# Kernel optimization log

Measured on AMD Instinct MI355X. Metric: run time of the kernel, lower is better.

## Reference

```python
import jax, jax.numpy as jnp
import numpy as np

N, E, F = 20000, 320000, 128
H = 2 * F  # MLP width = 256
EPS = 1e-5
TANH_ALPHA = 1.0


def setup_inputs() -> dict:
    key = jax.random.key(0)
    ks = jax.random.split(key, 16)
    x = jax.random.normal(ks[0], (N, F), dtype=jnp.float32)
    edge_index = jax.random.randint(ks[1], (2, E), 0, N, dtype=jnp.int64)
    s = 1.0 / np.sqrt(H)
    W1 = jax.random.uniform(ks[2], (H, H), jnp.float32, -s, s)
    b1 = jax.random.uniform(ks[3], (H,), jnp.float32, -s, s)
    g1 = jnp.ones((H,), jnp.float32)
    be1 = jnp.zeros((H,), jnp.float32)
    rm1 = jax.random.normal(ks[4], (H,), jnp.float32) * 0.1
    rv1 = jax.random.uniform(ks[5], (H,), jnp.float32, 0.5, 1.5)
    W2 = jax.random.uniform(ks[6], (H, H), jnp.float32, -s, s)
    b2 = jax.random.uniform(ks[7], (H,), jnp.float32, -s, s)
    g2 = jnp.ones((H,), jnp.float32)
    be2 = jnp.zeros((H,), jnp.float32)
    rm2 = jax.random.normal(ks[8], (H,), jnp.float32) * 0.1
    rv2 = jax.random.uniform(ks[9], (H,), jnp.float32, 0.5, 1.5)
    W3 = jax.random.uniform(ks[10], (F, H), jnp.float32, -s, s)
    b3 = jax.random.uniform(ks[11], (F,), jnp.float32, -s, s)
    return {"x": x, "edge_index": edge_index,
            "W1": W1, "b1": b1, "g1": g1, "be1": be1, "rm1": rm1, "rv1": rv1,
            "W2": W2, "b2": b2, "g2": g2, "be2": be2, "rm2": rm2, "rv2": rv2,
            "W3": W3, "b3": b3}


def _block(h, W, b, g, be, rm, rv):
    # Linear -> (Dropout inactive at eval) -> BatchNorm1d (eval, running stats) -> ReLU
    h = h @ W.T + b
    h = (h - rm) * (g * jax.lax.rsqrt(rv + EPS)) + be
    return jax.nn.relu(h)


def reference(x, edge_index, W1, b1, g1, be1, rm1, rv1,
              W2, b2, g2, be2, rm2, rv2, W3, b3):
    src, dst = edge_index[0], edge_index[1]  # PyG: x_j = x[src], x_i = x[dst]
    xi = x[dst]                              # [E, F]
    xj = x[src]                              # [E, F]
    h = jnp.concatenate([xi, xj - xi], axis=-1)  # [E, 2F]
    h = _block(h, W1, b1, g1, be1, rm1, rv1)
    h = _block(h, W2, b2, g2, be2, rm2, rv2)
    h = h @ W3.T + b3                        # [E, F]
    # scatter-mean aggregation over destination nodes
    summed = jax.ops.segment_sum(h, dst, num_segments=N)              # [N, F]
    cnt = jax.ops.segment_sum(jnp.ones((E,), h.dtype), dst, num_segments=N)
    agg = summed / jnp.maximum(cnt, 1.0)[:, None]
    return jnp.tanh(TANH_ALPHA * agg)
```

## Files before the change

kernel.cpp:

```cpp
#include <hip/hip_runtime.h>
#include <math.h>

#define NN 20000
#define EE 320000
#define FF 128
#define HH 256
#define MT 128

typedef _Float16 f16x8 __attribute__((ext_vector_type(8)));
typedef _Float16 f16x4 __attribute__((ext_vector_type(4)));
typedef float    f32x4  __attribute__((ext_vector_type(4)));
typedef float    f32x16 __attribute__((ext_vector_type(16)));

#define HADDR(m, bcol) (((m) << 9) + ((bcol) ^ (((m) & 7) << 4)))

#define WPTR_OFF  80000
#define SPAIR_OFF 160000
#define W2F_OFF   6560000
#define W3F_OFF   6691072
#define WCF_OFF   6756608
#define PQ_OFF    6887680

#define PB_HIST 1250
#define PB_W2   32
#define PB_WC   32
#define PB_W3   16
#define PREP_BLOCKS (PB_HIST + PB_W2 + PB_WC + PB_W3)

#define NODEB 313


__global__ __launch_bounds__(256) void prep_kernel(
    const int* __restrict__ eidx,
    const float* __restrict__ W1, const float* __restrict__ W2,
    const float* __restrict__ W3,
    _Float16* __restrict__ w2f, _Float16* __restrict__ wcf,
    _Float16* __restrict__ w3f, int* __restrict__ cnt)
{
    const int b = blockIdx.x, t = threadIdx.x;
    if (b < PB_HIST) {
        const int e = b * 256 + t;
        atomicAdd(&cnt[eidx[EE + e]], 1);
    } else if (b < PB_HIST + PB_W2) {
        const int f = (b - PB_HIST) * 256 + t;
        const int n = ((f >> 10) << 5) | (f & 31);
        const int k = (((f >> 6) & 15) << 4) | (((f >> 5) & 1) << 3);
        const float* s = W2 + (size_t)n * HH + k;
        _Float16 o[8];
        #pragma unroll
        for (int j = 0; j < 8; ++j) o[j] = (_Float16)s[j];
        __builtin_memcpy(w2f + (size_t)f * 8, o, 16);
    } else if (b < PB_HIST + PB_W2 + PB_WC) {
        const int f = (b - (PB_HIST + PB_W2)) * 256 + t;
        const int n = ((f >> 8) << 4) | (f & 15);
        const int k = (((f >> 6) & 3) << 5) | (((f >> 4) & 3) << 3);
        _Float16 o[8];
        if (n < HH) {
            const float* a = W1 + (size_t)n * HH + k;
            #pragma unroll
            for (int j = 0; j < 8; ++j) o[j] = (_Float16)(a[j] - a[FF + j]);
        } else {
            const float* a = W1 + (size_t)(n - HH) * HH + FF + k;
            #pragma unroll
            for (int j = 0; j < 8; ++j) o[j] = (_Float16)a[j];
        }
        __builtin_memcpy(wcf + (size_t)f * 8, o, 16);
    } else {
        const int f = (b - (PB_HIST + PB_W2 + PB_WC)) * 256 + t;
        const int n = ((f >> 10) << 5) | (f & 31);
        const int k = (((f >> 6) & 15) << 4) | (((f >> 5) & 1) << 3);
        const float* s = W3 + (size_t)n * HH + k;
        _Float16 o[8];
        #pragma unroll
        for (int j = 0; j < 8; ++j) o[j] = (_Float16)s[j];
        __builtin_memcpy(w3f + (size_t)f * 8, o, 16);
    }
}

__global__ __launch_bounds__(512) void node_kernel(
    const float* __restrict__ x, const _Float16* __restrict__ wcf,
    const float* __restrict__ b1, const float* __restrict__ g1,
    const float* __restrict__ be1, const float* __restrict__ rm1,
    const float* __restrict__ rv1,
    _Float16* __restrict__ PQ,
    const int* __restrict__ cnt, int* __restrict__ wptr)
{
    if (blockIdx.x == NODEB) {
        __shared__ int sp[512];
        const int t = threadIdx.x;
        const int base = t * 40;
        int s = 0;
        #pragma unroll 1
        for (int g = 0; g < 5; ++g) {
            int v[8];
            #pragma unroll
            for (int u = 0; u < 8; ++u) {
                const int idx = base + g * 8 + u;
                v[u] = (idx < NN) ? cnt[idx] : 0;
            }
            #pragma unroll
            for (int u = 0; u < 8; ++u) s += v[u];
        }
        sp[t] = s;
        __syncthreads();
        for (int d = 1; d < 512; d <<= 1) {
            const int v = (t >= d) ? sp[t - d] : 0;
            __syncthreads();
            sp[t] += v;
            __syncthreads();
        }
        int run = sp[t] - s;
        #pragma unroll 1
        for (int g = 0; g < 5; ++g) {
            int v[8];
            #pragma unroll
            for (int u = 0; u < 8; ++u) {
                const int idx = base + g * 8 + u;
                v[u] = (idx < NN) ? cnt[idx] : 0;
            }
            #pragma unroll
            for (int u = 0; u < 8; ++u) {
                const int idx = base + g * 8 + u;
                if (idx < NN) { wptr[idx] = run; run += v[u]; }
            }
        }
        return;
    }

    const int tid = threadIdx.x;
    const int lane = tid & 63, wv = tid >> 6;
    const int lr = lane & 15, lq = lane >> 4;
    const int node0 = blockIdx.x * 64;

    f32x4 acc[4][4];
    #pragma unroll
    for (int i = 0; i < 4; ++i)
        #pragma unroll
        for (int j = 0; j < 4; ++j) acc[i][j] = (f32x4){0.f, 0.f, 0.f, 0.f};

    const f16x8* wb = (const f16x8*)wcf + (size_t)(wv * 16) * 64 + lane;
    #pragma unroll 1
    for (int kb = 0; kb < 4; ++kb) {
        f16x8 wf[4], af[4];
        #pragma unroll
        for (int j = 0; j < 4; ++j) wf[j] = wb[(j * 4 + kb) * 64];
        #pragma unroll
        for (int i = 0; i < 4; ++i) {
            int nd = node0 + i * 16 + lr;
            if (nd > NN - 1) nd = NN - 1;
            const float* xp = x + (size_t)nd * FF + kb * 32 + lq * 8;
            const float4 xa = *(const float4*)xp;
            const float4 xb = *(const float4*)(xp + 4);
            f16x8 a;
            a[0] = (_Float16)xa.x; a[1] = (_Float16)xa.y;
            a[2] = (_Float16)xa.z; a[3] = (_Float16)xa.w;
            a[4] = (_Float16)xb.x; a[5] = (_Float16)xb.y;
            a[6] = (_Float16)xb.z; a[7] = (_Float16)xb.w;
            af[i] = a;
        }
        #pragma unroll
        for (int i = 0; i < 4; ++i)
            #pragma unroll
            for (int j = 0; j < 4; ++j)
                acc[i][j] = __builtin_amdgcn_mfma_f32_16x16x32_f16(wf[j], af[i], acc[i][j], 0, 0, 0);
    }

    #pragma unroll
    for (int j = 0; j < 4; ++j) {
        const int n0 = wv * 64 + j * 16 + lq * 4;
        const int ch = (n0 < HH) ? n0 : n0 - HH;
        float sc[4], cc[4];
        #pragma unroll
        for (int r = 0; r < 4; ++r) {
            const float s1 = g1[ch + r] * rsqrtf(rv1[ch + r] + 1e-5f);
            sc[r] = s1;
            cc[r] = (n0 < HH) ? (b1[ch + r] - rm1[ch + r]) * s1 + be1[ch + r] : 0.f;
        }
        #pragma unroll
        for (int i = 0; i < 4; ++i) {
            const int nd = node0 + i * 16 + lr;
            if (nd < NN) {
                f16x4 o;
                #pragma unroll
                for (int r = 0; r < 4; ++r) o[r] = (_Float16)(acc[i][j][r] * sc[r] + cc[r]);
                *(f16x4*)(PQ + (size_t)nd * 512 + n0) = o;
            }
        }
    }
}

__global__ __launch_bounds__(256) void scatter_kernel(const int* __restrict__ eidx,
                                                      int* __restrict__ wptr,
                                                      unsigned int* __restrict__ spair,
                                                      float* __restrict__ outp)
{
    const int idx = blockIdx.x * 256 + threadIdx.x;
    float4* o4 = (float4*)outp;
    #pragma unroll
    for (int i = 0; i < 2; ++i)
        o4[idx + i * 320000] = (float4){0.f, 0.f, 0.f, 0.f};
    if (idx < EE) {
        const int d = eidx[EE + idx];
        const int pos = atomicAdd(&wptr[d], 1);
        spair[pos] = (unsigned int)eidx[idx] | ((unsigned int)d << 16);
    }
}

__global__ __launch_bounds__(512, 4) void fused_edge_mlp(
    const _Float16* __restrict__ PQ,
    const unsigned int* __restrict__ spair,
    const _Float16* __restrict__ W2f,
    const float* __restrict__ b2, const float* __restrict__ g2,
    const float* __restrict__ be2, const float* __restrict__ rm2,
    const float* __restrict__ rv2,
    const _Float16* __restrict__ W3f,
    float* __restrict__ outp)
{
    __shared__ __align__(16) char shb[MT * 512];
    __shared__ __align__(16) float s_scale[HH];
    __shared__ __align__(16) float s_c[HH];
    __shared__ int s_dst[MT];

    const int tid = threadIdx.x;
    const int lane = tid & 63, wv = tid >> 6;
    const int lr = lane & 15, lq = lane >> 4;
    const int l5 = lane & 31, hf = lane >> 5;

    const int xcd = blockIdx.x & 7, bi = blockIdx.x >> 3;
    const int swz = (xcd < 4) ? (xcd * 313 + bi) : (1252 + (xcd - 4) * 312 + bi);
    const int e0 = swz * MT;

    {
        const int r = wv * 16 + lr;
        const int q = lq;
        const unsigned int pv = spair[e0 + r];
        const int dr = (int)(pv >> 16), sr = (int)(pv & 0xffffu);
        const f16x8* pd = (const f16x8*)(PQ + (size_t)dr * 512 + q * 64);
        const f16x8* ps = (const f16x8*)(PQ + (size_t)sr * 512 + 256 + q * 64);
        f16x8 av[8], bv[8];
        #pragma unroll
        for (int i = 0; i < 8; ++i) av[i] = pd[i];
        #pragma unroll
        for (int i = 0; i < 8; ++i) bv[i] = ps[i];

        if (tid < MT) s_dst[tid] = (int)(spair[e0 + tid] >> 16);
        if (tid < HH) {
            const float sc = g2[tid] * rsqrtf(rv2[tid] + 1e-5f);
            s_scale[tid] = sc;
            s_c[tid] = (b2[tid] - rm2[tid]) * sc + be2[tid];
        }

        #pragma unroll
        for (int i = 0; i < 8; ++i) {
            f16x8 s = av[i] + bv[i];
            f16x8 o;
            #pragma unroll
            for (int j = 0; j < 8; ++j) {
                const _Float16 z = (_Float16)0;
                o[j] = s[j] > z ? s[j] : z;
            }
            *(f16x8*)(shb + HADDR(r, q * 128 + i * 16)) = o;
        }
    }
    __syncthreads();

    {
        const int mt = wv & 3, nh = wv >> 2;
        const int m = mt * 32 + l5;
        f32x16 acc[4];
        const f32x16 zz = {};
        #pragma unroll
        for (int j = 0; j < 4; ++j) acc[j] = zz;

        const f16x8* wbase = (const f16x8*)W2f + lane;
        #pragma unroll 1
        for (int ks = 0; ks < 16; ++ks) {
            f16x8 wf[4];
            #pragma unroll
            for (int j = 0; j < 4; ++j)
                wf[j] = wbase[((nh * 4 + j) * 16 + ks) * 64];
            const f16x8 bf = *(const f16x8*)(shb + HADDR(m, ks * 32 + hf * 16));
            #pragma unroll
            for (int j = 0; j < 4; ++j)
                acc[j] = __builtin_amdgcn_mfma_f32_32x32x16_f16(wf[j], bf, acc[j], 0, 0, 0);
        }
        __syncthreads();
        #pragma unroll
        for (int j = 0; j < 4; ++j) {
            const int ntile = nh * 4 + j;
            #pragma unroll
            for (int grp = 0; grp < 4; ++grp) {
                const int n0 = ntile * 32 + grp * 8 + hf * 4;
                const float4 sc4 = *(const float4*)&s_scale[n0];
                const float4 cc4 = *(const float4*)&s_c[n0];
                f16x4 o;
                o[0] = (_Float16)fmaxf(acc[j][grp * 4 + 0] * sc4.x + cc4.x, 0.f);
                o[1] = (_Float16)fmaxf(acc[j][grp * 4 + 1] * sc4.y + cc4.y, 0.f);
                o[2] = (_Float16)fmaxf(acc[j][grp * 4 + 2] * sc4.z + cc4.z, 0.f);
                o[3] = (_Float16)fmaxf(acc[j][grp * 4 + 3] * sc4.w + cc4.w, 0.f);
                *(f16x4*)(shb + HADDR(m, n0 * 2)) = o;
            }
        }
        __syncthreads();
    }

    {
        const int mt = wv & 3, nh = wv >> 2;
        const int m = mt * 32 + l5;
        f32x16 acc[2];
        const f32x16 zz = {};
        acc[0] = zz; acc[1] = zz;

        const f16x8* wbase = (const f16x8*)W3f + lane;
        #pragma unroll 1
        for (int ks = 0; ks < 16; ++ks) {
            f16x8 wf[2];
            #pragma unroll
            for (int j = 0; j < 2; ++j)
                wf[j] = wbase[((nh * 2 + j) * 16 + ks) * 64];
            const f16x8 bf = *(const f16x8*)(shb + HADDR(m, ks * 32 + hf * 16));
            #pragma unroll
            for (int j = 0; j < 2; ++j)
                acc[j] = __builtin_amdgcn_mfma_f32_32x32x16_f16(wf[j], bf, acc[j], 0, 0, 0);
        }
        __syncthreads();
        #pragma unroll
        for (int j = 0; j < 2; ++j) {
            const int ntile = nh * 2 + j;
            #pragma unroll
            for (int grp = 0; grp < 4; ++grp) {
                const int n0 = ntile * 32 + grp * 8 + hf * 4;
                f32x4 o = { acc[j][grp * 4 + 0], acc[j][grp * 4 + 1],
                            acc[j][grp * 4 + 2], acc[j][grp * 4 + 3] };
                *(f32x4*)(shb + HADDR(m, n0 * 4)) = o;
            }
        }
        __syncthreads();

        {
            const int col = tid & 127;
            const int bc  = col * 4;
            const int r0  = (tid >> 7) * 32;
            int cur = s_dst[r0];
            float run = 0.f;
            #pragma unroll 1
            for (int g = 0; g < 4; ++g) {
                float v[8];
                #pragma unroll
                for (int u = 0; u < 8; ++u)
                    v[u] = *(const float*)(shb + HADDR(r0 + g * 8 + u, bc));
                #pragma unroll
                for (int u = 0; u < 8; ++u) {
                    const int r = r0 + g * 8 + u;
                    const int d = s_dst[r];
                    if (d != cur) {
                        atomicAdd(&outp[(size_t)cur * FF + col], run);
                        run = 0.f; cur = d;
                    }
                    run += v[u];
                }
            }
            atomicAdd(&outp[(size_t)cur * FF + col], run);
        }
    }
}

__global__ __launch_bounds__(256) void finalize_kernel(const int* __restrict__ cnt,
                                                       const float* __restrict__ b3,
                                                       float* __restrict__ out)
{
    const int i4 = (blockIdx.x * 256 + threadIdx.x) * 4;
    if (i4 < NN * FF) {
        const float c = fmaxf((float)cnt[i4 >> 7], 1.0f);
        const float rc = 1.0f / c;
        float4 v = *(const float4*)(out + i4);
        const float* bb = b3 + (i4 & 127);
        v.x = tanhf(v.x * rc + bb[0]);
        v.y = tanhf(v.y * rc + bb[1]);
        v.z = tanhf(v.z * rc + bb[2]);
        v.w = tanhf(v.w * rc + bb[3]);
        *(float4*)(out + i4) = v;
    }
}

extern "C" void kernel_launch(void* const* d_in, const int* in_sizes, int n_in,
                              void* d_out, int out_size, void* d_ws, size_t ws_size,
                              hipStream_t stream)
{
    const float* x   = (const float*)d_in[0];
    const int*   ei  = (const int*)d_in[1];
    const float* W1  = (const float*)d_in[2];
    const float* b1  = (const float*)d_in[3];
    const float* g1  = (const float*)d_in[4];
    const float* be1 = (const float*)d_in[5];
    const float* rm1 = (const float*)d_in[6];
    const float* rv1 = (const float*)d_in[7];
    const float* W2  = (const float*)d_in[8];
    const float* b2  = (const float*)d_in[9];
    const float* g2  = (const float*)d_in[10];
    const float* be2 = (const float*)d_in[11];
    const float* rm2 = (const float*)d_in[12];
    const float* rv2 = (const float*)d_in[13];
    const float* W3  = (const float*)d_in[14];
    const float* b3  = (const float*)d_in[15];

    char* ws = (char*)d_ws;
    int* cnt_i = (int*)ws;
    int* wptr  = (int*)(ws + WPTR_OFF);
    unsigned int* spair = (unsigned int*)(ws + SPAIR_OFF);
    _Float16* w2f = (_Float16*)(ws + W2F_OFF);
    _Float16* w3f = (_Float16*)(ws + W3F_OFF);
    _Float16* wcf = (_Float16*)(ws + WCF_OFF);
    _Float16* PQ  = (_Float16*)(ws + PQ_OFF);
    float* outp = (float*)d_out;

    hipMemsetAsync(cnt_i, 0, NN * sizeof(int), stream);

    prep_kernel<<<PREP_BLOCKS, 256, 0, stream>>>(ei, W1, W2, W3,
                                                 w2f, wcf, w3f, cnt_i);
    node_kernel<<<NODEB + 1, 512, 0, stream>>>(x, wcf, b1, g1, be1, rm1, rv1,
                                               PQ, cnt_i, wptr);
    scatter_kernel<<<(EE + 255) / 256, 256, 0, stream>>>(ei, wptr, spair, outp);
    fused_edge_mlp<<<EE / MT, 512, 0, stream>>>(PQ, spair,
                                                w2f, b2, g2, be2, rm2, rv2,
                                                w3f, outp);
    finalize_kernel<<<(NN * FF / 4 + 255) / 256, 256, 0, stream>>>(cnt_i, b3, outp);
}
```

Measured before the change: 304.6 us.

## Retile edge MLP GEMMs to 16x16x32 MFMA with 4x4 register blocking

Replaces the 32x32x16 MFMA tiling of the second and third layers with 16x16x32 MFMAs. Each wave now owns a 64x64 (layer 2) or 32x64 (layer 3) output block, so each LDS activation fragment is reused across four weight tiles and each weight fragment across several row tiles. The prep kernel writes W2 and W3 in a matching fragment layout. Weight fragments for the next k-block are prefetched in registers before the current block's MFMAs, to hide global load latency. This costs more accumulator registers, and the final prefetch reads one block past each weight buffer, which is harmless only because other buffers follow in the workspace.

```diff
diff --git a/kernel.cpp b/kernel.cpp
--- a/kernel.cpp
+++ b/kernel.cpp
@@ -9,8 +9,7 @@
 
 typedef _Float16 f16x8 __attribute__((ext_vector_type(8)));
 typedef _Float16 f16x4 __attribute__((ext_vector_type(4)));
-typedef float    f32x4  __attribute__((ext_vector_type(4)));
-typedef float    f32x16 __attribute__((ext_vector_type(16)));
+typedef float    f32x4 __attribute__((ext_vector_type(4)));
 
 #define HADDR(m, bcol) (((m) << 9) + ((bcol) ^ (((m) & 7) << 4)))
 
@@ -43,8 +42,8 @@
         atomicAdd(&cnt[eidx[EE + e]], 1);
     } else if (b < PB_HIST + PB_W2) {
         const int f = (b - PB_HIST) * 256 + t;
-        const int n = ((f >> 10) << 5) | (f & 31);
-        const int k = (((f >> 6) & 15) << 4) | (((f >> 5) & 1) << 3);
+        const int n = ((f >> 9) << 4) | (f & 15);
+        const int k = (((f >> 6) & 7) << 5) | (((f >> 4) & 3) << 3);
         const float* s = W2 + (size_t)n * HH + k;
         _Float16 o[8];
         #pragma unroll
@@ -67,8 +66,8 @@
         __builtin_memcpy(wcf + (size_t)f * 8, o, 16);
     } else {
         const int f = (b - (PB_HIST + PB_W2 + PB_WC)) * 256 + t;
-        const int n = ((f >> 10) << 5) | (f & 31);
-        const int k = (((f >> 6) & 15) << 4) | (((f >> 5) & 1) << 3);
+        const int n = ((f >> 9) << 4) | (f & 15);
+        const int k = (((f >> 6) & 7) << 5) | (((f >> 4) & 3) << 3);
         const float* s = W3 + (size_t)n * HH + k;
         _Float16 o[8];
         #pragma unroll
@@ -224,7 +223,6 @@
     const int tid = threadIdx.x;
     const int lane = tid & 63, wv = tid >> 6;
     const int lr = lane & 15, lq = lane >> 4;
-    const int l5 = lane & 31, hf = lane >> 5;
 
     const int xcd = blockIdx.x & 7, bi = blockIdx.x >> 3;
     const int swz = (xcd < 4) ? (xcd * 313 + bi) : (1252 + (xcd - 4) * 312 + bi);
@@ -265,39 +263,49 @@
     __syncthreads();
 
     {
-        const int mt = wv & 3, nh = wv >> 2;
-        const int m = mt * 32 + l5;
-        f32x16 acc[4];
-        const f32x16 zz = {};
-        #pragma unroll
-        for (int j = 0; j < 4; ++j) acc[j] = zz;
+        const int wm = wv >> 2, wn = wv & 3;
+        const int m_base = wm * 64;
+        f32x4 acc[4][4];
+        #pragma unroll
+        for (int i = 0; i < 4; ++i)
+            #pragma unroll
+            for (int j = 0; j < 4; ++j) acc[i][j] = (f32x4){0.f, 0.f, 0.f, 0.f};
 
         const f16x8* wbase = (const f16x8*)W2f + lane;
+        f16x8 cw[4];
+        #pragma unroll
+        for (int j = 0; j < 4; ++j) cw[j] = wbase[((wn * 4 + j) * 8) * 64];
         #pragma unroll 1
-        for (int ks = 0; ks < 16; ++ks) {
-            f16x8 wf[4];
-            #pragma unroll
-            for (int j = 0; j < 4; ++j)
-                wf[j] = wbase[((nh * 4 + j) * 16 + ks) * 64];
-            const f16x8 bf = *(const f16x8*)(shb + HADDR(m, ks * 32 + hf * 16));
-            #pragma unroll
-            for (int j = 0; j < 4; ++j)
-                acc[j] = __builtin_amdgcn_mfma_f32_32x32x16_f16(wf[j], bf, acc[j], 0, 0, 0);
+        for (int kb = 0; kb < 8; ++kb) {
+            f16x8 nw[4];
+            #pragma unroll
+            for (int j = 0; j < 4; ++j) nw[j] = wbase[((wn * 4 + j) * 8 + kb + 1) * 64];
+            f16x8 af[4];
+            #pragma unroll
+            for (int i = 0; i < 4; ++i)
+                af[i] = *(const f16x8*)(shb + HADDR(m_base + i * 16 + lr, kb * 64 + lq * 16));
+            #pragma unroll
+            for (int i = 0; i < 4; ++i)
+                #pragma unroll
+                for (int j = 0; j < 4; ++j)
+                    acc[i][j] = __builtin_amdgcn_mfma_f32_16x16x32_f16(cw[j], af[i], acc[i][j], 0, 0, 0);
+            #pragma unroll
+            for (int j = 0; j < 4; ++j) cw[j] = nw[j];
         }
         __syncthreads();
         #pragma unroll
         for (int j = 0; j < 4; ++j) {
-            const int ntile = nh * 4 + j;
-            #pragma unroll
-            for (int grp = 0; grp < 4; ++grp) {
-                const int n0 = ntile * 32 + grp * 8 + hf * 4;
-                const float4 sc4 = *(const float4*)&s_scale[n0];
-                const float4 cc4 = *(const float4*)&s_c[n0];
+            const int n0 = wn * 64 + j * 16 + lq * 4;
+            const float4 sc4 = *(const float4*)&s_scale[n0];
+            const float4 cc4 = *(const float4*)&s_c[n0];
+            #pragma unroll
+            for (int i = 0; i < 4; ++i) {
+                const int m = m_base + i * 16 + lr;
                 f16x4 o;
-                o[0] = (_Float16)fmaxf(acc[j][grp * 4 + 0] * sc4.x + cc4.x, 0.f);
-                o[1] = (_Float16)fmaxf(acc[j][grp * 4 + 1] * sc4.y + cc4.y, 0.f);
-                o[2] = (_Float16)fmaxf(acc[j][grp * 4 + 2] * sc4.z + cc4.z, 0.f);
-                o[3] = (_Float16)fmaxf(acc[j][grp * 4 + 3] * sc4.w + cc4.w, 0.f);
+                o[0] = (_Float16)fmaxf(acc[i][j][0] * sc4.x + cc4.x, 0.f);
+                o[1] = (_Float16)fmaxf(acc[i][j][1] * sc4.y + cc4.y, 0.f);
+                o[2] = (_Float16)fmaxf(acc[i][j][2] * sc4.z + cc4.z, 0.f);
+                o[3] = (_Float16)fmaxf(acc[i][j][3] * sc4.w + cc4.w, 0.f);
                 *(f16x4*)(shb + HADDR(m, n0 * 2)) = o;
             }
         }
@@ -305,34 +313,43 @@
     }
 
     {
-        const int mt = wv & 3, nh = wv >> 2;
-        const int m = mt * 32 + l5;
-        f32x16 acc[2];
-        const f32x16 zz = {};
-        acc[0] = zz; acc[1] = zz;
+        const int wm = wv >> 1, wn = wv & 1;
+        const int m_base = wm * 32;
+        f32x4 acc[2][4];
+        #pragma unroll
+        for (int i = 0; i < 2; ++i)
+            #pragma unroll
+            for (int j = 0; j < 4; ++j) acc[i][j] = (f32x4){0.f, 0.f, 0.f, 0.f};
 
         const f16x8* wbase = (const f16x8*)W3f + lane;
+        f16x8 cw[4];
+        #pragma unroll
+        for (int j = 0; j < 4; ++j) cw[j] = wbase[((wn * 4 + j) * 8) * 64];
         #pragma unroll 1
-        for (int ks = 0; ks < 16; ++ks) {
-            f16x8 wf[2];
-            #pragma unroll
-            for (int j = 0; j < 2; ++j)
-                wf[j] = wbase[((nh * 2 + j) * 16 + ks) * 64];
-            const f16x8 bf = *(const f16x8*)(shb + HADDR(m, ks * 32 + hf * 16));
-            #pragma unroll
-            for (int j = 0; j < 2; ++j)
-                acc[j] = __builtin_amdgcn_mfma_f32_32x32x16_f16(wf[j], bf, acc[j], 0, 0, 0);
+        for (int kb = 0; kb < 8; ++kb) {
+            f16x8 nw[4];
+            #pragma unroll
+            for (int j = 0; j < 4; ++j) nw[j] = wbase[((wn * 4 + j) * 8 + kb + 1) * 64];
+            f16x8 af[2];
+            #pragma unroll
+            for (int i = 0; i < 2; ++i)
+                af[i] = *(const f16x8*)(shb + HADDR(m_base + i * 16 + lr, kb * 64 + lq * 16));
+            #pragma unroll
+            for (int i = 0; i < 2; ++i)
+                #pragma unroll
+                for (int j = 0; j < 4; ++j)
+                    acc[i][j] = __builtin_amdgcn_mfma_f32_16x16x32_f16(cw[j], af[i], acc[i][j], 0, 0, 0);
+            #pragma unroll
+            for (int j = 0; j < 4; ++j) cw[j] = nw[j];
         }
         __syncthreads();
         #pragma unroll
-        for (int j = 0; j < 2; ++j) {
-            const int ntile = nh * 2 + j;
-            #pragma unroll
-            for (int grp = 0; grp < 4; ++grp) {
-                const int n0 = ntile * 32 + grp * 8 + hf * 4;
-                f32x4 o = { acc[j][grp * 4 + 0], acc[j][grp * 4 + 1],
-                            acc[j][grp * 4 + 2], acc[j][grp * 4 + 3] };
-                *(f32x4*)(shb + HADDR(m, n0 * 4)) = o;
+        for (int j = 0; j < 4; ++j) {
+            const int n0 = wn * 64 + j * 16 + lq * 4;
+            #pragma unroll
+            for (int i = 0; i < 2; ++i) {
+                const int m = m_base + i * 16 + lr;
+                *(f32x4*)(shb + HADDR(m, n0 * 4)) = acc[i][j];
             }
         }
         __syncthreads();
```

New measurement: 267.4 us. -12.2%, faster.

## Halve edge tile to 64 rows, prefetch weight fragments, raise MFMA priority

Applied to the files above, without the earlier changes.

The fused edge MLP kernel now works on 64-edge tiles with 256 threads (4 waves in a 2x2 M/N split) instead of 128-edge tiles with 512 threads. The LDS swizzle is widened and the block-to-XCD remap is simplified. The W2/W3 fragment loads are software-pipelined one k-step ahead, and s_setprio is raised around the MFMA loops. The node kernel also processes 32 nodes per block so that 625 blocks cover N exactly, which removes the bounds clamps. Smaller tiles mean more blocks and higher occupancy, but weights are reloaded from cache twice as often per edge, and the prefetch reads one step past each weight tile on the last iteration.

```diff
diff --git a/kernel.cpp b/kernel.cpp
--- a/kernel.cpp
+++ b/kernel.cpp
@@ -5,14 +5,15 @@
 #define EE 320000
 #define FF 128
 #define HH 256
-#define MT 128
+#define MT 64
+#define NTILE 5000
 
 typedef _Float16 f16x8 __attribute__((ext_vector_type(8)));
 typedef _Float16 f16x4 __attribute__((ext_vector_type(4)));
 typedef float    f32x4  __attribute__((ext_vector_type(4)));
 typedef float    f32x16 __attribute__((ext_vector_type(16)));
 
-#define HADDR(m, bcol) (((m) << 9) + ((bcol) ^ (((m) & 7) << 4)))
+#define HADDR(m, bcol) (((m) << 9) + ((bcol) ^ (((m) & 31) << 4)))
 
 #define WPTR_OFF  80000
 #define SPAIR_OFF 160000
@@ -27,7 +28,7 @@
 #define PB_W3   16
 #define PREP_BLOCKS (PB_HIST + PB_W2 + PB_WC + PB_W3)
 
-#define NODEB 313
+#define NODEB 625
 
 
 __global__ __launch_bounds__(256) void prep_kernel(
@@ -130,24 +131,23 @@
     const int tid = threadIdx.x;
     const int lane = tid & 63, wv = tid >> 6;
     const int lr = lane & 15, lq = lane >> 4;
-    const int node0 = blockIdx.x * 64;
-
-    f32x4 acc[4][4];
+    const int node0 = blockIdx.x * 32;
+
+    f32x4 acc[2][4];
     #pragma unroll
-    for (int i = 0; i < 4; ++i)
+    for (int i = 0; i < 2; ++i)
         #pragma unroll
         for (int j = 0; j < 4; ++j) acc[i][j] = (f32x4){0.f, 0.f, 0.f, 0.f};
 
     const f16x8* wb = (const f16x8*)wcf + (size_t)(wv * 16) * 64 + lane;
     #pragma unroll 1
     for (int kb = 0; kb < 4; ++kb) {
-        f16x8 wf[4], af[4];
+        f16x8 wf[4], af[2];
         #pragma unroll
         for (int j = 0; j < 4; ++j) wf[j] = wb[(j * 4 + kb) * 64];
         #pragma unroll
-        for (int i = 0; i < 4; ++i) {
-            int nd = node0 + i * 16 + lr;
-            if (nd > NN - 1) nd = NN - 1;
+        for (int i = 0; i < 2; ++i) {
+            const int nd = node0 + i * 16 + lr;
             const float* xp = x + (size_t)nd * FF + kb * 32 + lq * 8;
             const float4 xa = *(const float4*)xp;
             const float4 xb = *(const float4*)(xp + 4);
@@ -159,7 +159,7 @@
             af[i] = a;
         }
         #pragma unroll
-        for (int i = 0; i < 4; ++i)
+        for (int i = 0; i < 2; ++i)
             #pragma unroll
             for (int j = 0; j < 4; ++j)
                 acc[i][j] = __builtin_amdgcn_mfma_f32_16x16x32_f16(wf[j], af[i], acc[i][j], 0, 0, 0);
@@ -177,14 +177,12 @@
             cc[r] = (n0 < HH) ? (b1[ch + r] - rm1[ch + r]) * s1 + be1[ch + r] : 0.f;
         }
         #pragma unroll
-        for (int i = 0; i < 4; ++i) {
+        for (int i = 0; i < 2; ++i) {
             const int nd = node0 + i * 16 + lr;
-            if (nd < NN) {
-                f16x4 o;
-                #pragma unroll
-                for (int r = 0; r < 4; ++r) o[r] = (_Float16)(acc[i][j][r] * sc[r] + cc[r]);
-                *(f16x4*)(PQ + (size_t)nd * 512 + n0) = o;
-            }
+            f16x4 o;
+            #pragma unroll
+            for (int r = 0; r < 4; ++r) o[r] = (_Float16)(acc[i][j][r] * sc[r] + cc[r]);
+            *(f16x4*)(PQ + (size_t)nd * 512 + n0) = o;
         }
     }
 }
@@ -206,7 +204,7 @@
     }
 }
 
-__global__ __launch_bounds__(512, 4) void fused_edge_mlp(
+__global__ __launch_bounds__(256, 4) void fused_edge_mlp(
     const _Float16* __restrict__ PQ,
     const unsigned int* __restrict__ spair,
     const _Float16* __restrict__ W2f,
@@ -226,8 +224,7 @@
     const int lr = lane & 15, lq = lane >> 4;
     const int l5 = lane & 31, hf = lane >> 5;
 
-    const int xcd = blockIdx.x & 7, bi = blockIdx.x >> 3;
-    const int swz = (xcd < 4) ? (xcd * 313 + bi) : (1252 + (xcd - 4) * 312 + bi);
+    const int swz = (blockIdx.x & 7) * 625 + (blockIdx.x >> 3);
     const int e0 = swz * MT;
 
     {
@@ -244,7 +241,7 @@
         for (int i = 0; i < 8; ++i) bv[i] = ps[i];
 
         if (tid < MT) s_dst[tid] = (int)(spair[e0 + tid] >> 16);
-        if (tid < HH) {
+        {
             const float sc = g2[tid] * rsqrtf(rv2[tid] + 1e-5f);
             s_scale[tid] = sc;
             s_c[tid] = (b2[tid] - rm2[tid]) * sc + be2[tid];
@@ -265,29 +262,35 @@
     __syncthreads();
 
     {
-        const int mt = wv & 3, nh = wv >> 2;
-        const int m = mt * 32 + l5;
+        const int wm = wv >> 1, wn = wv & 1;
+        const int m = wm * 32 + l5;
         f32x16 acc[4];
         const f32x16 zz = {};
         #pragma unroll
         for (int j = 0; j < 4; ++j) acc[j] = zz;
 
         const f16x8* wbase = (const f16x8*)W2f + lane;
+        f16x8 cw[4];
+        #pragma unroll
+        for (int j = 0; j < 4; ++j) cw[j] = wbase[((wn * 4 + j) * 16) * 64];
+        __builtin_amdgcn_s_setprio(1);
         #pragma unroll 1
         for (int ks = 0; ks < 16; ++ks) {
-            f16x8 wf[4];
+            f16x8 nw[4];
+            #pragma unroll
+            for (int j = 0; j < 4; ++j) nw[j] = wbase[((wn * 4 + j) * 16 + ks + 1) * 64];
+            const f16x8 bf = *(const f16x8*)(shb + HADDR(m, ks * 32 + hf * 16));
             #pragma unroll
             for (int j = 0; j < 4; ++j)
-                wf[j] = wbase[((nh * 4 + j) * 16 + ks) * 64];
-            const f16x8 bf = *(const f16x8*)(shb + HADDR(m, ks * 32 + hf * 16));
-            #pragma unroll
-            for (int j = 0; j < 4; ++j)
-                acc[j] = __builtin_amdgcn_mfma_f32_32x32x16_f16(wf[j], bf, acc[j], 0, 0, 0);
-        }
+                acc[j] = __builtin_amdgcn_mfma_f32_32x32x16_f16(cw[j], bf, acc[j], 0, 0, 0);
+            #pragma unroll
+            for (int j = 0; j < 4; ++j) cw[j] = nw[j];
+        }
+        __builtin_amdgcn_s_setprio(0);
         __syncthreads();
         #pragma unroll
         for (int j = 0; j < 4; ++j) {
-            const int ntile = nh * 4 + j;
+            const int ntile = wn * 4 + j;
             #pragma unroll
             for (int grp = 0; grp < 4; ++grp) {
                 const int n0 = ntile * 32 + grp * 8 + hf * 4;
@@ -305,28 +308,34 @@
     }
 
     {
-        const int mt = wv & 3, nh = wv >> 2;
-        const int m = mt * 32 + l5;
+        const int wm = wv >> 1, wn = wv & 1;
+        const int m = wm * 32 + l5;
         f32x16 acc[2];
         const f32x16 zz = {};
         acc[0] = zz; acc[1] = zz;
 
         const f16x8* wbase = (const f16x8*)W3f + lane;
+        f16x8 cw[2];
+        #pragma unroll
+        for (int j = 0; j < 2; ++j) cw[j] = wbase[((wn * 2 + j) * 16) * 64];
+        __builtin_amdgcn_s_setprio(1);
         #pragma unroll 1
         for (int ks = 0; ks < 16; ++ks) {
-            f16x8 wf[2];
+            f16x8 nw[2];
+            #pragma unroll
+            for (int j = 0; j < 2; ++j) nw[j] = wbase[((wn * 2 + j) * 16 + ks + 1) * 64];
+            const f16x8 bf = *(const f16x8*)(shb + HADDR(m, ks * 32 + hf * 16));
             #pragma unroll
             for (int j = 0; j < 2; ++j)
-                wf[j] = wbase[((nh * 2 + j) * 16 + ks) * 64];
-            const f16x8 bf = *(const f16x8*)(shb + HADDR(m, ks * 32 + hf * 16));
-            #pragma unroll
-            for (int j = 0; j < 2; ++j)
-                acc[j] = __builtin_amdgcn_mfma_f32_32x32x16_f16(wf[j], bf, acc[j], 0, 0, 0);
-        }
+                acc[j] = __builtin_amdgcn_mfma_f32_32x32x16_f16(cw[j], bf, acc[j], 0, 0, 0);
+            #pragma unroll
+            for (int j = 0; j < 2; ++j) cw[j] = nw[j];
+        }
+        __builtin_amdgcn_s_setprio(0);
         __syncthreads();
         #pragma unroll
         for (int j = 0; j < 2; ++j) {
-            const int ntile = nh * 2 + j;
+            const int ntile = wn * 2 + j;
             #pragma unroll
             for (int grp = 0; grp < 4; ++grp) {
                 const int n0 = ntile * 32 + grp * 8 + hf * 4;
@@ -421,8 +430,8 @@
     node_kernel<<<NODEB + 1, 512, 0, stream>>>(x, wcf, b1, g1, be1, rm1, rv1,
                                                PQ, cnt_i, wptr);
     scatter_kernel<<<(EE + 255) / 256, 256, 0, stream>>>(ei, wptr, spair, outp);
-    fused_edge_mlp<<<EE / MT, 512, 0, stream>>>(PQ, spair,
-                                                w2f, b2, g2, be2, rm2, rv2,
-                                                w3f, outp);
+    fused_edge_mlp<<<NTILE, 256, 0, stream>>>(PQ, spair,
+                                              w2f, b2, g2, be2, rm2, rv2,
+                                              w3f, outp);
     finalize_kernel<<<(NN * FF / 4 + 255) / 256, 256, 0, stream>>>(cnt_i, b3, outp);
 }
```

New measurement: 281.4 us. 7.6% less time.
